# Optimization experiments

Hardware: AMD Instinct MI355X
Metric: run time of the kernel (lower is better)

Reference implementation:

```python
import itertools
import jax, jax.numpy as jnp
import numpy as np

B, S, D = 256, 49, 448          # batch, tokens (7x7), channels
H, KD, ED = 8, 32, 128          # heads, key_dim, expanded_key_dim (attn_ratio*key_dim)
QKV_OUT = H * (KD + KD + ED)    # 1536
MLP_HID = 4 * D                 # 1792
EPS = 1e-12
SCALE = KD ** -0.5


def _bias_idxs(resolution=7):
    points = list(itertools.product(range(resolution), range(resolution)))
    offsets, idxs = {}, []
    for p1 in points:
        for p2 in points:
            off = (abs(p1[0] - p2[0]), abs(p1[1] - p2[1]))
            if off not in offsets:
                offsets[off] = len(offsets)
            idxs.append(offsets[off])
    n = len(points)
    return np.asarray(idxs, np.int32).reshape(n, n), len(offsets)


def setup_inputs() -> dict:
    key = jax.random.key(0)
    ks = jax.random.split(key, 12)
    idxs_np, n_off = _bias_idxs(7)  # [49,49], 49 offsets
    s = 0.02
    return {
        "hidden_states": jax.random.normal(ks[0], (B, S, D), jnp.float32),
        "ln2_w": jnp.ones((D,), jnp.float32),
        "ln2_b": jnp.zeros((D,), jnp.float32),
        "qkv_w": jax.random.normal(ks[1], (QKV_OUT, D), jnp.float32) * s,
        "qkv_b": jnp.zeros((QKV_OUT,), jnp.float32),
        "proj_w": jax.random.normal(ks[2], (D, H * ED), jnp.float32) * s,
        "proj_b": jnp.zeros((D,), jnp.float32),
        "attention_biases": jax.random.normal(ks[3], (H, n_off), jnp.float32) * s,
        "fc1_w": jax.random.normal(ks[4], (MLP_HID, D), jnp.float32) * s,
        "fc1_b": jnp.zeros((MLP_HID,), jnp.float32),
        "fc2_w": jax.random.normal(ks[5], (D, MLP_HID), jnp.float32) * s,
        "fc2_b": jnp.zeros((D,), jnp.float32),
        "layer_scale_1": jnp.full((D,), 1e-5, jnp.float32),
        "layer_scale_2": jnp.full((D,), 1e-5, jnp.float32),
        "attention_bias_idxs": jnp.asarray(idxs_np),  # int32 [49,49]
    }


def _layernorm(x, w, b):
    mu = jnp.mean(x, axis=-1, keepdims=True)
    var = jnp.mean(jnp.square(x - mu), axis=-1, keepdims=True)
    return (x - mu) * jax.lax.rsqrt(var + EPS) * w + b


def reference(hidden_states, ln2_w, ln2_b, qkv_w, qkv_b, proj_w, proj_b,
              attention_biases, fc1_w, fc1_b, fc2_w, fc2_b,
              layer_scale_1, layer_scale_2, attention_bias_idxs):
    # NOTE: upstream code applies norm2 before BOTH attention and MLP (faithful).
    norm = _layernorm(hidden_states, ln2_w, ln2_b)  # [B,S,D]

    qkv = (norm @ qkv_w.T + qkv_b).reshape(B, S, H, KD + KD + ED)
    q, k, v = jnp.split(qkv, [KD, 2 * KD], axis=-1)  # [B,S,H,KD/KD/ED]

    bias = attention_biases[:, attention_bias_idxs]  # [H,S,S] gathered rel-pos bias
    scores = jnp.einsum("bqhd,bkhd->bhqk", q, k) * SCALE + bias[None]
    probs = jax.nn.softmax(scores, axis=-1)          # [B,H,S,S]

    ctx = jnp.einsum("bhqk,bkhd->bqhd", probs, v).reshape(B, S, H * ED)
    attn_out = ctx @ proj_w.T + proj_b               # [B,S,D]

    out = hidden_states + layer_scale_1 * attn_out
    mlp = jax.nn.gelu(norm @ fc1_w.T + fc1_b, approximate=False) @ fc2_w.T + fc2_b
    out = out + layer_scale_2 * mlp
    return out
```

## Files before the change

kernel.cpp:

```cpp
#include <hip/hip_runtime.h>
#include <hip/hip_bf16.h>
#include <cstdint>

#define B_    256
#define S_    49
#define D_    448
#define H_    8
#define NTOK  (B_*S_)
#define QKVO  1536
#define MLPH  1792
#define SCALE_ 0.17677669529663687f

using bf16x8  = __attribute__((ext_vector_type(8))) __bf16;
using ushort8 = __attribute__((ext_vector_type(8))) unsigned short;
using f32x4   = __attribute__((ext_vector_type(4))) float;

__device__ __forceinline__ unsigned short f2bf(float f){
  uint32_t u = __builtin_bit_cast(uint32_t, f);
  u += 0x7fffu + ((u >> 16) & 1u);
  return (unsigned short)(u >> 16);
}
__device__ __forceinline__ float b2f(unsigned short b){
  uint32_t u = ((uint32_t)b) << 16;
  return __builtin_bit_cast(float, u);
}

__device__ __forceinline__ void gload_lds16(const void* g, void* l){
  __builtin_amdgcn_global_load_lds(
      (const __attribute__((address_space(1))) void*)g,
      (__attribute__((address_space(3))) void*)l, 16, 0, 0);
}

#define P_S0 688128L
#define P_S1 1490944L
#define P_S2 1949696L
#define P_S3 2752512L
#define P_S4 2932736L
#define P_S5 2936064L
#define P_S6 2936576L
#define P_S7 2969344L
__global__ __launch_bounds__(256)
void prep_k(const float* __restrict__ qkvw, const float* __restrict__ fc1w,
            const float* __restrict__ projw, const float* __restrict__ fc2w,
            const float* __restrict__ ls1, const float* __restrict__ ls2,
            const float* __restrict__ qkvb, const float* __restrict__ fc1b,
            const float* __restrict__ projb, const float* __restrict__ fc2b,
            const float* __restrict__ attb, const int* __restrict__ idxs,
            unsigned short* __restrict__ wcat, unsigned short* __restrict__ wfused,
            float* __restrict__ cbig, float* __restrict__ cbv,
            float* __restrict__ biasf){
  const long i = (long)blockIdx.x * 256 + threadIdx.x;
  if (i < P_S0){
    wcat[i] = f2bf(qkvw[i]);
  } else if (i < P_S1){
    long j = i - P_S0;
    wcat[i] = f2bf(fc1w[j]);
  } else if (i < P_S2){
    long j = i - P_S1;
    long r = j / 1024, c = j - r*1024;
    wfused[r*2816 + c] = f2bf(projw[j]*ls1[r]);
  } else if (i < P_S3){
    long j = i - P_S2;
    long r = j / 1792, c = j - r*1792;
    wfused[r*2816 + 1024 + c] = f2bf(fc2w[j]*ls2[r]);
  } else if (i < P_S4){
    long j = i - P_S3;
    wfused[448L*2816 + j] = 0;
  } else if (i < P_S5){
    long j = i - P_S4;
    cbig[j] = (j < 1536) ? qkvb[j] : fc1b[j - 1536];
  } else if (i < P_S6){
    long j = i - P_S5;
    cbv[j] = (j < 448) ? ls1[j]*projb[j] + ls2[j]*fc2b[j] : 0.f;
  } else if (i < P_S7){
    long j = i - P_S6;
    int h = (int)(j >> 12), r = (int)((j >> 6) & 63), c = (int)(j & 63);
    float v;
    if (c >= 49) v = -1e30f;
    else { int q = r < 49 ? r : 48; v = attb[h*49 + idxs[q*49 + c]]; }
    biasf[j] = v;
  }
}

__global__ __launch_bounds__(448)
void ln_k(const float* __restrict__ x, const float* __restrict__ w,
          const float* __restrict__ b, unsigned short* __restrict__ out){
  const int tok = blockIdx.x, t = threadIdx.x;
  const float v = x[(size_t)tok*448 + t];
  float s1 = v, s2 = v*v;
  #pragma unroll
  for (int o = 32; o; o >>= 1){ s1 += __shfl_xor(s1, o); s2 += __shfl_xor(s2, o); }
  __shared__ float a1[7], a2[7];
  const int wid = t >> 6;
  if ((t & 63) == 0){ a1[wid] = s1; a2[wid] = s2; }
  __syncthreads();
  float S1 = 0.f, S2 = 0.f;
  #pragma unroll
  for (int i = 0; i < 7; ++i){ S1 += a1[i]; S2 += a2[i]; }
  const float mu  = S1 * (1.f/448.f);
  const float var = S2 * (1.f/448.f) - mu*mu;
  const float rs  = rsqrtf(var + 1e-12f);
  out[(size_t)tok*448 + t] = f2bf((v - mu)*rs*w[t] + b[t]);
}

template<int EPI>
__global__ __launch_bounds__(256)
void gemm_k(const unsigned short* __restrict__ A1, int lda1, int nkt1,
            const unsigned short* __restrict__ A2, int lda2, int nkt,
            const unsigned short* __restrict__ W, int ldw,
            const float* __restrict__ bias,
            const float* __restrict__ resid, float* __restrict__ outF,
            unsigned short* __restrict__ outB1, int ldo1,
            unsigned short* __restrict__ outB2, int ldo2,
            int splitBy, int nby)
{
  constexpr int BN = (EPI == 4) ? 128 : 64;
  constexpr int NF = BN/32;
  __shared__ char smem[32768];

  const int NB = gridDim.x;
  const int q8 = NB >> 3, r8 = NB & 7;
  const int xcd = blockIdx.x & 7, idx = blockIdx.x >> 3;
  const int wgid = (xcd < r8 ? xcd*(q8+1) : r8*(q8+1) + (xcd-r8)*q8) + idx;
  const int bx = wgid / nby, by = wgid - bx*nby;

  const int t = threadIdx.x, lane = t & 63, wid = t >> 6;
  const int wm = wid >> 1, wn = wid & 1;
  const int g = lane >> 4, li = lane & 15;
  f32x4 acc[4][NF] = {};

  const int l3   = lane >> 3;
  const int sp   = (lane & 7) ^ l3;
  const int rofs = 2*l3 + (sp >> 2);
  const int cofs = (sp & 3)*8;

  auto stage = [&](int buf, int kt){
    char* Asb = smem + buf*8192;
    char* Bsb = smem + 16384 + buf*(BN*64);
    const unsigned short* Ab; int lda, k0;
    if (kt < nkt1){ Ab = A1; lda = lda1; k0 = kt*32; }
    else          { Ab = A2; lda = lda2; k0 = (kt - nkt1)*32; }
    #pragma unroll
    for (int i = 0; i < 2; ++i){
      const int c = wid*2 + i;
      gload_lds16(Ab + (size_t)(bx*128 + c*16 + rofs)*lda + k0 + cofs,
                  Asb + c*1024);
    }
    if (BN == 128){
      #pragma unroll
      for (int i = 0; i < 2; ++i){
        const int c = wid*2 + i;
        gload_lds16(W + (size_t)(by*BN + c*16 + rofs)*ldw + kt*32 + cofs,
                    Bsb + c*1024);
      }
    } else {
      gload_lds16(W + (size_t)(by*BN + wid*16 + rofs)*ldw + kt*32 + cofs,
                  Bsb + wid*1024);
    }
  };

  const int sOff = (li >> 1)*128 + ((((li & 1)*4 + g) ^ (li >> 1)) << 4);

  int buf = 0;
  stage(0, 0);
  for (int kt = 0; kt < nkt; ++kt){
    __syncthreads();
    if (kt + 1 < nkt) stage(buf ^ 1, kt + 1);
    char* Asb = smem + buf*8192;
    char* Bsb = smem + 16384 + buf*(BN*64);
    bf16x8 af[4], bfr[NF];
    #pragma unroll
    for (int mf = 0; mf < 4; ++mf)
      af[mf] = *reinterpret_cast<const bf16x8*>(Asb + wm*4096 + mf*1024 + sOff);
    #pragma unroll
    for (int nf = 0; nf < NF; ++nf)
      bfr[nf] = *reinterpret_cast<const bf16x8*>(Bsb + wn*(BN*32) + nf*1024 + sOff);
    #pragma unroll
    for (int mf = 0; mf < 4; ++mf)
      #pragma unroll
      for (int nf = 0; nf < NF; ++nf)
        acc[mf][nf] = __builtin_amdgcn_mfma_f32_16x16x32_bf16(af[mf], bfr[nf], acc[mf][nf], 0, 0, 0);
    buf ^= 1;
  }
  __syncthreads();

  const int lr = lane >> 4, lc = lane & 15;
  if (EPI == 4){
    const bool dogelu = by >= splitBy;
    #pragma unroll
    for (int p = 0; p < 2; ++p){
      if (p) __syncthreads();
      if (wm == p){
        #pragma unroll
        for (int mf = 0; mf < 4; ++mf){
          #pragma unroll
          for (int nf = 0; nf < NF; ++nf){
            const int col = wn*64 + nf*16 + li;
            const float bi = bias[by*128 + col];
            #pragma unroll
            for (int j = 0; j < 4; ++j){
              const int rt = mf*16 + g*4 + j;
              float v = acc[mf][nf][j] + bi;
              if (dogelu) v = 0.5f*v*(1.0f + erff(v*0.70710678118654752f));
              *reinterpret_cast<float*>(smem + rt*512 + ((col*4) ^ (((rt >> 2) & 3) << 6))) = v;
            }
          }
        }
      }
      __syncthreads();
      #pragma unroll
      for (int it = 0; it < 4; ++it){
        const int rt = wid*16 + it*4 + lr;
        const int sw = ((rt >> 2) & 3) << 6;
        const f32x4 v0 = *reinterpret_cast<const f32x4*>(smem + rt*512 + ((lc*32)      ^ sw));
        const f32x4 v1 = *reinterpret_cast<const f32x4*>(smem + rt*512 + ((lc*32 + 16) ^ sw));
        ushort8 u;
        #pragma unroll
        for (int k = 0; k < 4; ++k){ u[k] = f2bf(v0[k]); u[4+k] = f2bf(v1[k]); }
        const int grow = bx*128 + p*64 + rt;
        if (by < splitBy)
          *reinterpret_cast<ushort8*>(outB1 + (size_t)grow*ldo1 + by*128 + lc*8) = u;
        else
          *reinterpret_cast<ushort8*>(outB2 + (size_t)grow*ldo2 + (by - splitBy)*128 + lc*8) = u;
      }
    }
  } else {
    #pragma unroll
    for (int mf = 0; mf < 4; ++mf){
      #pragma unroll
      for (int nf = 0; nf < NF; ++nf){
        const int col = wn*32 + nf*16 + li;
        const float bi = bias[by*64 + col];
        #pragma unroll
        for (int j = 0; j < 4; ++j){
          const int rt = wm*64 + mf*16 + g*4 + j;
          *reinterpret_cast<float*>(smem + rt*256 + ((col*4) ^ (((rt >> 2) & 1) << 6)))
              = acc[mf][nf][j] + bi;
        }
      }
    }
    __syncthreads();
    #pragma unroll
    for (int i = 0; i < 8; ++i){
      const int r = wid*32 + i*4 + lr;
      const int sw = ((r >> 2) & 1) << 6;
      const f32x4 v = *reinterpret_cast<const f32x4*>(smem + r*256 + ((lc*16) ^ sw));
      const size_t o = (size_t)(bx*128 + r)*448 + by*64 + lc*4;
      const f32x4 rs = *reinterpret_cast<const f32x4*>(resid + o);
      *reinterpret_cast<f32x4*>(outF + o) = rs + v;
    }
  }
}

__global__ __launch_bounds__(256)
void attn_mfma_k(const unsigned short* __restrict__ qkv,
                 const float* __restrict__ biasf,
                 unsigned short* __restrict__ ctx)
{
  const int bh = blockIdx.x;
  const int b = bh >> 3, h = bh & 7;
  __shared__ unsigned short Vs[64*128];
  __shared__ unsigned short Ps[64*64];
  const int t = threadIdx.x, lane = t & 63, w = t >> 6;
  const int g = lane >> 4, li = lane & 15;
  const size_t qbase = ((size_t)b*49)*QKVO + (size_t)h*192;

  for (int c = t; c < 64*16; c += 256){
    const int k = c >> 4, seg = c & 15;
    bf16x8 v = {};
    if (k < 49)
      v = *reinterpret_cast<const bf16x8*>(qkv + qbase + 64 + (size_t)k*QKVO + seg*8);
    const int byte = (k*256 + seg*16) ^ ((((unsigned)k >> 3) & 3) << 5);
    *reinterpret_cast<bf16x8*>((char*)Vs + byte) = v;
  }

  const int qrow = w*16 + li;
  bf16x8 afq = {};
  if (qrow < 49)
    afq = *reinterpret_cast<const bf16x8*>(qkv + qbase + (size_t)qrow*QKVO + g*8);
  f32x4 accs[4];
  #pragma unroll
  for (int nf = 0; nf < 4; ++nf){
    const int krow = nf*16 + li;
    bf16x8 bfr = {};
    if (krow < 49)
      bfr = *reinterpret_cast<const bf16x8*>(qkv + qbase + 32 + (size_t)krow*QKVO + g*8);
    f32x4 z = {};
    accs[nf] = __builtin_amdgcn_mfma_f32_16x16x32_bf16(afq, bfr, z, 0, 0, 0);
  }

  #pragma unroll
  for (int j = 0; j < 4; ++j){
    const int row = w*16 + g*4 + j;
    float sv[4];
    #pragma unroll
    for (int nf = 0; nf < 4; ++nf)
      sv[nf] = accs[nf][j]*SCALE_ + biasf[h*4096 + row*64 + nf*16 + li];
    float m = fmaxf(fmaxf(sv[0], sv[1]), fmaxf(sv[2], sv[3]));
    #pragma unroll
    for (int o = 8; o; o >>= 1) m = fmaxf(m, __shfl_xor(m, o));
    float e[4], s = 0.f;
    #pragma unroll
    for (int nf = 0; nf < 4; ++nf){ e[nf] = __expf(sv[nf] - m); s += e[nf]; }
    #pragma unroll
    for (int o = 8; o; o >>= 1) s += __shfl_xor(s, o);
    const float inv = 1.f / s;
    #pragma unroll
    for (int nf = 0; nf < 4; ++nf){
      const int byte = (row*128 + (nf*16 + li)*2) ^ ((row & 7) << 4);
      *reinterpret_cast<unsigned short*>((char*)Ps + byte) = f2bf(e[nf]*inv);
    }
  }
  __syncthreads();

  f32x4 accp[4][2] = {};
  #pragma unroll
  for (int kt = 0; kt < 2; ++kt){
    bf16x8 pa[4];
    #pragma unroll
    for (int mt = 0; mt < 4; ++mt){
      const int q = mt*16 + li;
      const int byte = (q*128 + kt*64 + g*16) ^ ((q & 7) << 4);
      pa[mt] = *reinterpret_cast<const bf16x8*>((char*)Ps + byte);
    }
    #pragma unroll
    for (int nf = 0; nf < 2; ++nf){
      const int d = w*32 + nf*16 + li;
      ushort8 vbu;
      #pragma unroll
      for (int j = 0; j < 8; ++j){
        const int k = kt*32 + g*8 + j;
        const int byte = (k*256 + d*2) ^ ((((unsigned)k >> 3) & 3) << 5);
        vbu[j] = *reinterpret_cast<const unsigned short*>((char*)Vs + byte);
      }
      const bf16x8 vb = __builtin_bit_cast(bf16x8, vbu);
      #pragma unroll
      for (int mt = 0; mt < 4; ++mt)
        accp[mt][nf] = __builtin_amdgcn_mfma_f32_16x16x32_bf16(pa[mt], vb, accp[mt][nf], 0, 0, 0);
    }
  }

  const size_t obase = ((size_t)b*49)*1024 + (size_t)h*128;
  #pragma unroll
  for (int mt = 0; mt < 4; ++mt){
    #pragma unroll
    for (int nf = 0; nf < 2; ++nf){
      #pragma unroll
      for (int j = 0; j < 4; ++j){
        const int row = mt*16 + g*4 + j;
        if (row < 49){
          const int col = w*32 + nf*16 + li;
          ctx[obase + (size_t)row*1024 + col] = f2bf(accp[mt][nf][j]);
        }
      }
    }
  }
}

extern "C" void kernel_launch(void* const* d_in, const int* in_sizes, int n_in,
                              void* d_out, int out_size, void* d_ws, size_t ws_size,
                              hipStream_t stream)
{
  const float* hidden = (const float*)d_in[0];
  const float* ln2w   = (const float*)d_in[1];
  const float* ln2b   = (const float*)d_in[2];
  const float* qkvw   = (const float*)d_in[3];
  const float* qkvb   = (const float*)d_in[4];
  const float* projw  = (const float*)d_in[5];
  const float* projb  = (const float*)d_in[6];
  const float* attb   = (const float*)d_in[7];
  const float* fc1w   = (const float*)d_in[8];
  const float* fc1b   = (const float*)d_in[9];
  const float* fc2w   = (const float*)d_in[10];
  const float* fc2b   = (const float*)d_in[11];
  const float* ls1    = (const float*)d_in[12];
  const float* ls2    = (const float*)d_in[13];
  const int*   aidx   = (const int*)d_in[14];
  float* out = (float*)d_out;

  char* p = (char*)d_ws;
  auto alloc = [&](size_t bytes){ void* r = (void*)p; p += (bytes + 255) & ~(size_t)255; return r; };
  unsigned short* wcat   = (unsigned short*)alloc((size_t)3328*448*2);
  unsigned short* wfused = (unsigned short*)alloc((size_t)512*2816*2);
  unsigned short* normb  = (unsigned short*)alloc((size_t)NTOK*448*2);
  unsigned short* qkvv   = (unsigned short*)alloc((size_t)NTOK*QKVO*2);
  unsigned short* ctx    = (unsigned short*)alloc((size_t)NTOK*1024*2);
  unsigned short* hid    = (unsigned short*)alloc((size_t)NTOK*MLPH*2);
  float*          biasf  = (float*)alloc((size_t)8*64*64*4);
  float*          cbig   = (float*)alloc((size_t)3328*4);
  float*          cbv    = (float*)alloc((size_t)512*4);

  prep_k<<<(int)(P_S7/256), 256, 0, stream>>>(qkvw, fc1w, projw, fc2w, ls1, ls2,
                                              qkvb, fc1b, projb, fc2b, attb, aidx,
                                              wcat, wfused, cbig, cbv, biasf);
  ln_k<<<NTOK, 448, 0, stream>>>(hidden, ln2w, ln2b, normb);

  gemm_k<4><<<98*26, 256, 0, stream>>>(normb, 448, 14, nullptr, 448, 14,
                                       wcat, 448, cbig,
                                       nullptr, nullptr,
                                       qkvv, QKVO, hid, MLPH, 12, 26);
  attn_mfma_k<<<B_*H_, 256, 0, stream>>>(qkvv, biasf, ctx);
  gemm_k<1><<<98*7, 256, 0, stream>>>(ctx, 1024, 32, hid, MLPH, 88,
                                      wfused, 2816, cbv,
                                      hidden, out,
                                      nullptr, 0, nullptr, 0, 999, 7);
}
```

Before: 181.6 us.

## Use single-buffered 64-wide K tiles in GEMM instead of double-buffered 32

The GEMM kernel now stages 64-wide K slices into one shared buffer with an XOR swizzle on 128-byte rows, replacing the double-buffered 32-wide slices. Each iteration runs two MFMA k-substeps, then syncs and issues the next load. Trip counts are halved at the launch sites. This halves the number of barriers and loop iterations per K, but the next tile's loads no longer overlap the current tile's MFMAs, which exposes global load latency.

```diff
diff --git a/kernel.cpp b/kernel.cpp
--- a/kernel.cpp
+++ b/kernel.cpp
@@ -117,6 +117,8 @@
   constexpr int BN = (EPI == 4) ? 128 : 64;
   constexpr int NF = BN/32;
   __shared__ char smem[32768];
+  unsigned short* const As = (unsigned short*)smem;
+  unsigned short* const Bs = (unsigned short*)(smem + 16384);
 
   const int NB = gridDim.x;
   const int q8 = NB >> 3, r8 = NB & 7;
@@ -129,58 +131,54 @@
   const int g = lane >> 4, li = lane & 15;
   f32x4 acc[4][NF] = {};
 
-  const int l3   = lane >> 3;
-  const int sp   = (lane & 7) ^ l3;
-  const int rofs = 2*l3 + (sp >> 2);
-  const int cofs = (sp & 3)*8;
-
-  auto stage = [&](int buf, int kt){
-    char* Asb = smem + buf*8192;
-    char* Bsb = smem + 16384 + buf*(BN*64);
+  const int srow  = lane >> 3;
+  const int scolw = ((lane & 7) ^ srow) * 8;
+
+  auto stage = [&](int kt){
     const unsigned short* Ab; int lda, k0;
-    if (kt < nkt1){ Ab = A1; lda = lda1; k0 = kt*32; }
-    else          { Ab = A2; lda = lda2; k0 = (kt - nkt1)*32; }
-    #pragma unroll
-    for (int i = 0; i < 2; ++i){
-      const int c = wid*2 + i;
-      gload_lds16(Ab + (size_t)(bx*128 + c*16 + rofs)*lda + k0 + cofs,
-                  Asb + c*1024);
-    }
-    if (BN == 128){
-      #pragma unroll
-      for (int i = 0; i < 2; ++i){
-        const int c = wid*2 + i;
-        gload_lds16(W + (size_t)(by*BN + c*16 + rofs)*ldw + kt*32 + cofs,
-                    Bsb + c*1024);
-      }
-    } else {
-      gload_lds16(W + (size_t)(by*BN + wid*16 + rofs)*ldw + kt*32 + cofs,
-                  Bsb + wid*1024);
+    if (kt < nkt1){ Ab = A1; lda = lda1; k0 = kt*64; }
+    else          { Ab = A2; lda = lda2; k0 = (kt - nkt1)*64; }
+    #pragma unroll
+    for (int i = 0; i < 4; ++i){
+      const int c = wid*4 + i;
+      gload_lds16(Ab + (size_t)(bx*128 + c*8 + srow)*lda + k0 + scolw, As + c*512);
+    }
+    #pragma unroll
+    for (int i = 0; i < NF; ++i){
+      const int c = wid*NF + i;
+      gload_lds16(W + (size_t)(by*BN + c*8 + srow)*ldw + kt*64 + scolw, Bs + c*512);
     }
   };
 
-  const int sOff = (li >> 1)*128 + ((((li & 1)*4 + g) ^ (li >> 1)) << 4);
-
-  int buf = 0;
-  stage(0, 0);
+  stage(0);
   for (int kt = 0; kt < nkt; ++kt){
     __syncthreads();
-    if (kt + 1 < nkt) stage(buf ^ 1, kt + 1);
-    char* Asb = smem + buf*8192;
-    char* Bsb = smem + 16384 + buf*(BN*64);
-    bf16x8 af[4], bfr[NF];
-    #pragma unroll
-    for (int mf = 0; mf < 4; ++mf)
-      af[mf] = *reinterpret_cast<const bf16x8*>(Asb + wm*4096 + mf*1024 + sOff);
-    #pragma unroll
-    for (int nf = 0; nf < NF; ++nf)
-      bfr[nf] = *reinterpret_cast<const bf16x8*>(Bsb + wn*(BN*32) + nf*1024 + sOff);
-    #pragma unroll
-    for (int mf = 0; mf < 4; ++mf)
-      #pragma unroll
-      for (int nf = 0; nf < NF; ++nf)
-        acc[mf][nf] = __builtin_amdgcn_mfma_f32_16x16x32_bf16(af[mf], bfr[nf], acc[mf][nf], 0, 0, 0);
-    buf ^= 1;
+    #pragma unroll
+    for (int ks = 0; ks < 2; ++ks){
+      const int kk2 = (ks*32 + g*8)*2;
+      bf16x8 af[4], bfr[NF];
+      #pragma unroll
+      for (int mf = 0; mf < 4; ++mf){
+        const int row = wm*64 + mf*16 + li;
+        af[mf] = *reinterpret_cast<const bf16x8*>(
+            (char*)As + row*128 + (kk2 ^ ((row & 7) << 4)));
+      }
+      #pragma unroll
+      for (int nf = 0; nf < NF; ++nf){
+        const int row = wn*(BN/2) + nf*16 + li;
+        bfr[nf] = *reinterpret_cast<const bf16x8*>(
+            (char*)Bs + row*128 + (kk2 ^ ((row & 7) << 4)));
+      }
+      #pragma unroll
+      for (int mf = 0; mf < 4; ++mf)
+        #pragma unroll
+        for (int nf = 0; nf < NF; ++nf)
+          acc[mf][nf] = __builtin_amdgcn_mfma_f32_16x16x32_bf16(af[mf], bfr[nf], acc[mf][nf], 0, 0, 0);
+    }
+    if (kt + 1 < nkt){
+      __syncthreads();
+      stage(kt + 1);
+    }
   }
   __syncthreads();
 
@@ -395,12 +393,12 @@
                                               wcat, wfused, cbig, cbv, biasf);
   ln_k<<<NTOK, 448, 0, stream>>>(hidden, ln2w, ln2b, normb);
 
-  gemm_k<4><<<98*26, 256, 0, stream>>>(normb, 448, 14, nullptr, 448, 14,
+  gemm_k<4><<<98*26, 256, 0, stream>>>(normb, 448, 7, nullptr, 448, 7,
                                        wcat, 448, cbig,
                                        nullptr, nullptr,
                                        qkvv, QKVO, hid, MLPH, 12, 26);
   attn_mfma_k<<<B_*H_, 256, 0, stream>>>(qkvv, biasf, ctx);
-  gemm_k<1><<<98*7, 256, 0, stream>>>(ctx, 1024, 32, hid, MLPH, 88,
+  gemm_k<1><<<98*7, 256, 0, stream>>>(ctx, 1024, 16, hid, MLPH, 44,
                                       wfused, 2816, cbv,
                                       hidden, out,
                                       nullptr, 0, nullptr, 0, 999, 7);
```

New measurement: 188.9 us. 1.04x slower.

## Triple-buffer GEMM loads with vmcnt waits and specialize GEMM kernels

Applied to the files above, without the earlier changes.

Splits the templated GEMM into two specialized kernels with compile-time loop counts and strides. Each switches from double buffering with a full __syncthreads to a three-stage LDS ring that prefetches two k-tiles ahead, using explicit s_waitcnt vmcnt plus s_barrier so loads overlap more compute. The QKV/fc1 epilogue now writes the whole 128x128 tile to 64KB of LDS in one pass instead of two halves. The larger LDS footprint (64KB, 36KB) can lower occupancy, and the hand-counted vmcnt values must match the number of outstanding loads per stage.

```diff
diff --git a/kernel.cpp b/kernel.cpp
--- a/kernel.cpp
+++ b/kernel.cpp
@@ -103,20 +103,15 @@
   out[(size_t)tok*448 + t] = f2bf((v - mu)*rs*w[t] + b[t]);
 }
 
-template<int EPI>
 __global__ __launch_bounds__(256)
-void gemm_k(const unsigned short* __restrict__ A1, int lda1, int nkt1,
-            const unsigned short* __restrict__ A2, int lda2, int nkt,
-            const unsigned short* __restrict__ W, int ldw,
-            const float* __restrict__ bias,
-            const float* __restrict__ resid, float* __restrict__ outF,
-            unsigned short* __restrict__ outB1, int ldo1,
-            unsigned short* __restrict__ outB2, int ldo2,
-            int splitBy, int nby)
+void gemm4_k(const unsigned short* __restrict__ A,
+             const unsigned short* __restrict__ W,
+             const float* __restrict__ bias,
+             unsigned short* __restrict__ outB1,
+             unsigned short* __restrict__ outB2,
+             int splitBy, int nby)
 {
-  constexpr int BN = (EPI == 4) ? 128 : 64;
-  constexpr int NF = BN/32;
-  __shared__ char smem[32768];
+  __shared__ char smem[65536];
 
   const int NB = gridDim.x;
   const int q8 = NB >> 3, r8 = NB & 7;
@@ -127,7 +122,7 @@
   const int t = threadIdx.x, lane = t & 63, wid = t >> 6;
   const int wm = wid >> 1, wn = wid & 1;
   const int g = lane >> 4, li = lane & 15;
-  f32x4 acc[4][NF] = {};
+  f32x4 acc[4][4] = {};
 
   const int l3   = lane >> 3;
   const int sp   = (lane & 7) ^ l3;
@@ -135,120 +130,178 @@
   const int cofs = (sp & 3)*8;
 
   auto stage = [&](int buf, int kt){
-    char* Asb = smem + buf*8192;
-    char* Bsb = smem + 16384 + buf*(BN*64);
+    char* Asb = smem + buf*16384;
+    char* Bsb = Asb + 8192;
+    const int k0 = kt*32;
+    #pragma unroll
+    for (int i = 0; i < 2; ++i){
+      const int c = wid*2 + i;
+      gload_lds16(A + (size_t)(bx*128 + c*16 + rofs)*448 + k0 + cofs, Asb + c*1024);
+    }
+    #pragma unroll
+    for (int i = 0; i < 2; ++i){
+      const int c = wid*2 + i;
+      gload_lds16(W + (size_t)(by*128 + c*16 + rofs)*448 + k0 + cofs, Bsb + c*1024);
+    }
+  };
+
+  const int sOff = (li >> 1)*128 + ((((li & 1)*4 + g) ^ (li >> 1)) << 4);
+
+  stage(0, 0);
+  stage(1, 1);
+  int cur = 0, stg = 2;
+  for (int kt = 0; kt < 14; ++kt){
+    if (kt < 13) asm volatile("s_waitcnt vmcnt(4)" ::: "memory");
+    else         asm volatile("s_waitcnt vmcnt(0)" ::: "memory");
+    __builtin_amdgcn_s_barrier();
+    if (kt + 2 < 14){ stage(stg, kt + 2); stg = (stg == 2) ? 0 : stg + 1; }
+    char* Asb = smem + cur*16384;
+    char* Bsb = Asb + 8192;
+    bf16x8 af[4], bfr[4];
+    #pragma unroll
+    for (int mf = 0; mf < 4; ++mf)
+      af[mf] = *reinterpret_cast<const bf16x8*>(Asb + (wm*4 + mf)*1024 + sOff);
+    #pragma unroll
+    for (int nf = 0; nf < 4; ++nf)
+      bfr[nf] = *reinterpret_cast<const bf16x8*>(Bsb + (wn*4 + nf)*1024 + sOff);
+    #pragma unroll
+    for (int mf = 0; mf < 4; ++mf)
+      #pragma unroll
+      for (int nf = 0; nf < 4; ++nf)
+        acc[mf][nf] = __builtin_amdgcn_mfma_f32_16x16x32_bf16(af[mf], bfr[nf], acc[mf][nf], 0, 0, 0);
+    cur = (cur == 2) ? 0 : cur + 1;
+  }
+  __syncthreads();
+
+  const bool dogelu = by >= splitBy;
+  #pragma unroll
+  for (int mf = 0; mf < 4; ++mf){
+    #pragma unroll
+    for (int nf = 0; nf < 4; ++nf){
+      const int col = wn*64 + nf*16 + li;
+      const float bi = bias[by*128 + col];
+      #pragma unroll
+      for (int j = 0; j < 4; ++j){
+        const int row = wm*64 + mf*16 + g*4 + j;
+        float v = acc[mf][nf][j] + bi;
+        if (dogelu) v = 0.5f*v*(1.0f + erff(v*0.70710678118654752f));
+        *reinterpret_cast<float*>(smem + row*512 + ((col*4) ^ (((row >> 2) & 3) << 6))) = v;
+      }
+    }
+  }
+  __syncthreads();
+  const int lr = lane >> 4, lc = lane & 15;
+  #pragma unroll
+  for (int it = 0; it < 8; ++it){
+    const int r = wid*32 + it*4 + lr;
+    const int sw = ((r >> 2) & 3) << 6;
+    const f32x4 v0 = *reinterpret_cast<const f32x4*>(smem + r*512 + ((lc*32)      ^ sw));
+    const f32x4 v1 = *reinterpret_cast<const f32x4*>(smem + r*512 + ((lc*32 + 16) ^ sw));
+    ushort8 u;
+    #pragma unroll
+    for (int k = 0; k < 4; ++k){ u[k] = f2bf(v0[k]); u[4+k] = f2bf(v1[k]); }
+    const int grow = bx*128 + r;
+    if (by < splitBy)
+      *reinterpret_cast<ushort8*>(outB1 + (size_t)grow*QKVO + by*128 + lc*8) = u;
+    else
+      *reinterpret_cast<ushort8*>(outB2 + (size_t)grow*MLPH + (by - splitBy)*128 + lc*8) = u;
+  }
+}
+
+__global__ __launch_bounds__(256)
+void gemm1_k(const unsigned short* __restrict__ A1,
+             const unsigned short* __restrict__ A2,
+             const unsigned short* __restrict__ W,
+             const float* __restrict__ bias,
+             const float* __restrict__ resid, float* __restrict__ outF,
+             int nby)
+{
+  __shared__ char smem[36864];
+
+  const int NB = gridDim.x;
+  const int q8 = NB >> 3, r8 = NB & 7;
+  const int xcd = blockIdx.x & 7, idx = blockIdx.x >> 3;
+  const int wgid = (xcd < r8 ? xcd*(q8+1) : r8*(q8+1) + (xcd-r8)*q8) + idx;
+  const int bx = wgid / nby, by = wgid - bx*nby;
+
+  const int t = threadIdx.x, lane = t & 63, wid = t >> 6;
+  const int wm = wid >> 1, wn = wid & 1;
+  const int g = lane >> 4, li = lane & 15;
+  f32x4 acc[4][2] = {};
+
+  const int l3   = lane >> 3;
+  const int sp   = (lane & 7) ^ l3;
+  const int rofs = 2*l3 + (sp >> 2);
+  const int cofs = (sp & 3)*8;
+
+  auto stage = [&](int buf, int kt){
+    char* Asb = smem + buf*12288;
+    char* Bsb = Asb + 8192;
     const unsigned short* Ab; int lda, k0;
-    if (kt < nkt1){ Ab = A1; lda = lda1; k0 = kt*32; }
-    else          { Ab = A2; lda = lda2; k0 = (kt - nkt1)*32; }
+    if (kt < 32){ Ab = A1; lda = 1024; k0 = kt*32; }
+    else        { Ab = A2; lda = 1792; k0 = (kt - 32)*32; }
     #pragma unroll
     for (int i = 0; i < 2; ++i){
       const int c = wid*2 + i;
       gload_lds16(Ab + (size_t)(bx*128 + c*16 + rofs)*lda + k0 + cofs,
                   Asb + c*1024);
     }
-    if (BN == 128){
-      #pragma unroll
-      for (int i = 0; i < 2; ++i){
-        const int c = wid*2 + i;
-        gload_lds16(W + (size_t)(by*BN + c*16 + rofs)*ldw + kt*32 + cofs,
-                    Bsb + c*1024);
+    gload_lds16(W + (size_t)(by*64 + wid*16 + rofs)*2816 + kt*32 + cofs,
+                Bsb + wid*1024);
+  };
+
+  const int sOff = (li >> 1)*128 + ((((li & 1)*4 + g) ^ (li >> 1)) << 4);
+
+  stage(0, 0);
+  stage(1, 1);
+  int cur = 0, stg = 2;
+  for (int kt = 0; kt < 88; ++kt){
+    if (kt < 87) asm volatile("s_waitcnt vmcnt(3)" ::: "memory");
+    else         asm volatile("s_waitcnt vmcnt(0)" ::: "memory");
+    __builtin_amdgcn_s_barrier();
+    if (kt + 2 < 88){ stage(stg, kt + 2); stg = (stg == 2) ? 0 : stg + 1; }
+    char* Asb = smem + cur*12288;
+    char* Bsb = Asb + 8192;
+    bf16x8 af[4], bfr[2];
+    #pragma unroll
+    for (int mf = 0; mf < 4; ++mf)
+      af[mf] = *reinterpret_cast<const bf16x8*>(Asb + (wm*4 + mf)*1024 + sOff);
+    #pragma unroll
+    for (int nf = 0; nf < 2; ++nf)
+      bfr[nf] = *reinterpret_cast<const bf16x8*>(Bsb + (wn*2 + nf)*1024 + sOff);
+    #pragma unroll
+    for (int mf = 0; mf < 4; ++mf)
+      #pragma unroll
+      for (int nf = 0; nf < 2; ++nf)
+        acc[mf][nf] = __builtin_amdgcn_mfma_f32_16x16x32_bf16(af[mf], bfr[nf], acc[mf][nf], 0, 0, 0);
+    cur = (cur == 2) ? 0 : cur + 1;
+  }
+  __syncthreads();
+
+  #pragma unroll
+  for (int mf = 0; mf < 4; ++mf){
+    #pragma unroll
+    for (int nf = 0; nf < 2; ++nf){
+      const int col = wn*32 + nf*16 + li;
+      const float bi = bias[by*64 + col];
+      #pragma unroll
+      for (int j = 0; j < 4; ++j){
+        const int rt = wm*64 + mf*16 + g*4 + j;
+        *reinterpret_cast<float*>(smem + rt*256 + ((col*4) ^ (((rt >> 2) & 1) << 6)))
+            = acc[mf][nf][j] + bi;
       }
-    } else {
-      gload_lds16(W + (size_t)(by*BN + wid*16 + rofs)*ldw + kt*32 + cofs,
-                  Bsb + wid*1024);
-    }
-  };
-
-  const int sOff = (li >> 1)*128 + ((((li & 1)*4 + g) ^ (li >> 1)) << 4);
-
-  int buf = 0;
-  stage(0, 0);
-  for (int kt = 0; kt < nkt; ++kt){
-    __syncthreads();
-    if (kt + 1 < nkt) stage(buf ^ 1, kt + 1);
-    char* Asb = smem + buf*8192;
-    char* Bsb = smem + 16384 + buf*(BN*64);
-    bf16x8 af[4], bfr[NF];
-    #pragma unroll
-    for (int mf = 0; mf < 4; ++mf)
-      af[mf] = *reinterpret_cast<const bf16x8*>(Asb + wm*4096 + mf*1024 + sOff);
-    #pragma unroll
-    for (int nf = 0; nf < NF; ++nf)
-      bfr[nf] = *reinterpret_cast<const bf16x8*>(Bsb + wn*(BN*32) + nf*1024 + sOff);
-    #pragma unroll
-    for (int mf = 0; mf < 4; ++mf)
-      #pragma unroll
-      for (int nf = 0; nf < NF; ++nf)
-        acc[mf][nf] = __builtin_amdgcn_mfma_f32_16x16x32_bf16(af[mf], bfr[nf], acc[mf][nf], 0, 0, 0);
-    buf ^= 1;
-  }
-  __syncthreads();
-
+    }
+  }
+  __syncthreads();
   const int lr = lane >> 4, lc = lane & 15;
-  if (EPI == 4){
-    const bool dogelu = by >= splitBy;
-    #pragma unroll
-    for (int p = 0; p < 2; ++p){
-      if (p) __syncthreads();
-      if (wm == p){
-        #pragma unroll
-        for (int mf = 0; mf < 4; ++mf){
-          #pragma unroll
-          for (int nf = 0; nf < NF; ++nf){
-            const int col = wn*64 + nf*16 + li;
-            const float bi = bias[by*128 + col];
-            #pragma unroll
-            for (int j = 0; j < 4; ++j){
-              const int rt = mf*16 + g*4 + j;
-              float v = acc[mf][nf][j] + bi;
-              if (dogelu) v = 0.5f*v*(1.0f + erff(v*0.70710678118654752f));
-              *reinterpret_cast<float*>(smem + rt*512 + ((col*4) ^ (((rt >> 2) & 3) << 6))) = v;
-            }
-          }
-        }
-      }
-      __syncthreads();
-      #pragma unroll
-      for (int it = 0; it < 4; ++it){
-        const int rt = wid*16 + it*4 + lr;
-        const int sw = ((rt >> 2) & 3) << 6;
-        const f32x4 v0 = *reinterpret_cast<const f32x4*>(smem + rt*512 + ((lc*32)      ^ sw));
-        const f32x4 v1 = *reinterpret_cast<const f32x4*>(smem + rt*512 + ((lc*32 + 16) ^ sw));
-        ushort8 u;
-        #pragma unroll
-        for (int k = 0; k < 4; ++k){ u[k] = f2bf(v0[k]); u[4+k] = f2bf(v1[k]); }
-        const int grow = bx*128 + p*64 + rt;
-        if (by < splitBy)
-          *reinterpret_cast<ushort8*>(outB1 + (size_t)grow*ldo1 + by*128 + lc*8) = u;
-        else
-          *reinterpret_cast<ushort8*>(outB2 + (size_t)grow*ldo2 + (by - splitBy)*128 + lc*8) = u;
-      }
-    }
-  } else {
-    #pragma unroll
-    for (int mf = 0; mf < 4; ++mf){
-      #pragma unroll
-      for (int nf = 0; nf < NF; ++nf){
-        const int col = wn*32 + nf*16 + li;
-        const float bi = bias[by*64 + col];
-        #pragma unroll
-        for (int j = 0; j < 4; ++j){
-          const int rt = wm*64 + mf*16 + g*4 + j;
-          *reinterpret_cast<float*>(smem + rt*256 + ((col*4) ^ (((rt >> 2) & 1) << 6)))
-              = acc[mf][nf][j] + bi;
-        }
-      }
-    }
-    __syncthreads();
-    #pragma unroll
-    for (int i = 0; i < 8; ++i){
-      const int r = wid*32 + i*4 + lr;
-      const int sw = ((r >> 2) & 1) << 6;
-      const f32x4 v = *reinterpret_cast<const f32x4*>(smem + r*256 + ((lc*16) ^ sw));
-      const size_t o = (size_t)(bx*128 + r)*448 + by*64 + lc*4;
-      const f32x4 rs = *reinterpret_cast<const f32x4*>(resid + o);
-      *reinterpret_cast<f32x4*>(outF + o) = rs + v;
-    }
+  #pragma unroll
+  for (int i = 0; i < 8; ++i){
+    const int r = wid*32 + i*4 + lr;
+    const int sw = ((r >> 2) & 1) << 6;
+    const f32x4 v = *reinterpret_cast<const f32x4*>(smem + r*256 + ((lc*16) ^ sw));
+    const size_t o = (size_t)(bx*128 + r)*448 + by*64 + lc*4;
+    const f32x4 rs = *reinterpret_cast<const f32x4*>(resid + o);
+    *reinterpret_cast<f32x4*>(outF + o) = rs + v;
   }
 }
 
@@ -395,13 +448,8 @@
                                               wcat, wfused, cbig, cbv, biasf);
   ln_k<<<NTOK, 448, 0, stream>>>(hidden, ln2w, ln2b, normb);
 
-  gemm_k<4><<<98*26, 256, 0, stream>>>(normb, 448, 14, nullptr, 448, 14,
-                                       wcat, 448, cbig,
-                                       nullptr, nullptr,
-                                       qkvv, QKVO, hid, MLPH, 12, 26);
+  gemm4_k<<<98*26, 256, 0, stream>>>(normb, wcat, cbig, qkvv, hid, 12, 26);
   attn_mfma_k<<<B_*H_, 256, 0, stream>>>(qkvv, biasf, ctx);
-  gemm_k<1><<<98*7, 256, 0, stream>>>(ctx, 1024, 32, hid, MLPH, 88,
-                                      wfused, 2816, cbv,
-                                      hidden, out,
-                                      nullptr, 0, nullptr, 0, 999, 7);
-}
+  gemm1_k<<<98*7, 256, 0, stream>>>(ctx, hid, wfused, cbv,
+                                    hidden, out, 7);
+}
```

Measured after the change: 171.1 us. -5.8%, faster.
